# Kernel tuning notes

Hardware: AMD Instinct MI355X
Metric: run time of the kernel (lower is better)

## Reference

```python
import jax, jax.numpy as jnp
import numpy as np


def _pairwise_dist(x):
    # Euclidean (p=2) pairwise distance matrix with a safe sqrt (zero diag).
    sq = jnp.sum(x * x, axis=1)
    d2 = sq[:, None] + sq[None, :] - 2.0 * (x @ x.T)
    d2 = jnp.maximum(d2, 0.0)
    safe = jnp.where(d2 > 0, d2, 1.0)
    return jnp.where(d2 > 0, jnp.sqrt(safe), 0.0)


def _mst_pairs(D):
    # 0-dim Vietoris-Rips persistence pairs == MST edges of the distance graph.
    # Prim's algorithm, vectorized per step via lax.scan (n-1 sequential steps).
    n = D.shape[0]
    D = jax.lax.stop_gradient(D)  # pairing indices are discrete
    inf = jnp.array(jnp.inf, D.dtype)
    idx = jnp.arange(n)
    min_dist = jnp.where(idx == 0, inf, D[0])  # start tree at node 0
    parent = jnp.zeros((n,), dtype=jnp.int32)

    def step(carry, _):
        min_dist, parent = carry
        j = jnp.argmin(min_dist)
        edge = jnp.stack([parent[j], j.astype(jnp.int32)])
        cand = D[j]
        upd = cand < min_dist
        parent = jnp.where(upd, j.astype(jnp.int32), parent)
        min_dist = jnp.minimum(min_dist, cand)
        min_dist = min_dist.at[j].set(inf)
        return (min_dist, parent), edge

    _, edges = jax.lax.scan(step, (min_dist, parent), None, length=n - 1)
    return edges  # [n-1, 2] int32


def setup_inputs() -> dict:
    key = jax.random.key(0)
    kx, kz = jax.random.split(key)
    x = jax.random.normal(kx, (4096, 3072), dtype=jnp.float32)
    z = jax.random.normal(kz, (4096, 128), dtype=jnp.float32)
    return {"x": x, "z": z}


def reference(x, z):
    x = x.astype(jnp.float32)
    z = z.astype(jnp.float32)
    Dx = _pairwise_dist(x)
    Dz = _pairwise_dist(z)
    px = _mst_pairs(Dx)  # persistence pairing of the data space
    pz = _mst_pairs(Dz)  # persistence pairing of the latent space
    dx_px = Dx[px[:, 0], px[:, 1]]
    dz_px = Dz[px[:, 0], px[:, 1]]
    dx_pz = Dx[pz[:, 0], pz[:, 1]]
    dz_pz = Dz[pz[:, 0], pz[:, 1]]
    # Signature matching loss (Moor et al. 2020), p=2:
    # 0.5*||d_X[pi_X] - d_Z[pi_X]||^2 + 0.5*||d_X[pi_Z] - d_Z[pi_Z]||^2
    return 0.5 * jnp.sum((dx_px - dz_px) ** 2) + 0.5 * jnp.sum((dx_pz - dz_pz) ** 2)
```

## Files before the change

kernel.cpp:

```cpp
#include <hip/hip_runtime.h>
#include <hip/hip_fp16.h>

#define N 4096
#define KX 3072
#define KZ 128
#define NBT (N / 128)
#define NTRI2 (NBT * (NBT + 1) / 2)

typedef __attribute__((ext_vector_type(8))) short bf16x8;
typedef __attribute__((ext_vector_type(4))) float f32x4;

__device__ __forceinline__ short f2bf(float f) {
  unsigned u = __float_as_uint(f);
  u += 0x7fffu + ((u >> 16) & 1u);
  return (short)(u >> 16);
}

__device__ __forceinline__ unsigned umin2(unsigned a, unsigned b) { return a < b ? a : b; }

template <int CTRL>
__device__ __forceinline__ unsigned dpp_umin(unsigned x) {
  unsigned y = (unsigned)__builtin_amdgcn_update_dpp(0, (int)x, CTRL, 0xF, 0xF, true);
  return umin2(x, y);
}

__global__ __launch_bounds__(256) void cvt_bf16_kernel(const float* __restrict__ X,
                                                       short* __restrict__ Xb, int n8) {
  int stride = gridDim.x * 256;
  for (int i = blockIdx.x * 256 + threadIdx.x; i < n8; i += stride) {
    float4 a = *(const float4*)(X + (size_t)i * 8);
    float4 b = *(const float4*)(X + (size_t)i * 8 + 4);
    bf16x8 o;
    o[0] = f2bf(a.x); o[1] = f2bf(a.y); o[2] = f2bf(a.z); o[3] = f2bf(a.w);
    o[4] = f2bf(b.x); o[5] = f2bf(b.y); o[6] = f2bf(b.z); o[7] = f2bf(b.w);
    *(bf16x8*)(Xb + (size_t)i * 8) = o;
  }
}

__global__ __launch_bounds__(256) void sqnorm_kernel(const float* __restrict__ X, int K,
                                                     float* __restrict__ sq) {
  int row = blockIdx.x;
  const float4* xr = (const float4*)(X + (size_t)row * K);
  float s = 0.f;
  int n4 = K >> 2;
  for (int i = threadIdx.x; i < n4; i += 256) {
    float4 v = xr[i];
    s += v.x * v.x + v.y * v.y + v.z * v.z + v.w * v.w;
  }
  for (int off = 32; off > 0; off >>= 1) s += __shfl_down(s, off);
  __shared__ float wsum[4];
  int lane = threadIdx.x & 63, w = threadIdx.x >> 6;
  if (lane == 0) wsum[w] = s;
  __syncthreads();
  if (threadIdx.x == 0) {
    float t = 0.f;
    #pragma unroll
    for (int i = 0; i < 4; ++i) t += wsum[i];
    sq[row] = t;
  }
}

__global__ __launch_bounds__(256) void dist_mfma_kernel(const short* __restrict__ Xb, int K,
                                                        const float* __restrict__ sq,
                                                        __half* __restrict__ D) {
  int t = blockIdx.x;
  int br = (int)((sqrtf(8.0f * (float)t + 1.0f) - 1.0f) * 0.5f);
  while ((br + 1) * (br + 2) / 2 <= t) ++br;
  while (br * (br + 1) / 2 > t) --br;
  int bc = t - br * (br + 1) / 2;
  int i0 = br * 128, j0 = bc * 128;

  __shared__ short As[128][40];
  __shared__ short Bs[128][40];

  int tid = threadIdx.x, lane = tid & 63, w = tid >> 6;
  int wr = w >> 1, wc = w & 1;
  int fr = lane & 15, fc = lane >> 4;

  f32x4 acc[4][4];
  #pragma unroll
  for (int m = 0; m < 4; ++m)
    #pragma unroll
    for (int nn = 0; nn < 4; ++nn)
      acc[m][nn] = (f32x4){0.f, 0.f, 0.f, 0.f};

  for (int k0 = 0; k0 < K; k0 += 32) {
    #pragma unroll
    for (int u = 0; u < 2; ++u) {
      int f = tid + u * 256;
      int r = f >> 2;
      int c = (f & 3) * 8;
      *(bf16x8*)&As[r][c] = *(const bf16x8*)(Xb + (size_t)(i0 + r) * K + k0 + c);
      *(bf16x8*)&Bs[r][c] = *(const bf16x8*)(Xb + (size_t)(j0 + r) * K + k0 + c);
    }
    __syncthreads();
    bf16x8 af[4], bg[4];
    #pragma unroll
    for (int m = 0; m < 4; ++m)
      af[m] = *(const bf16x8*)&As[wr * 64 + m * 16 + fr][fc * 8];
    #pragma unroll
    for (int nn = 0; nn < 4; ++nn)
      bg[nn] = *(const bf16x8*)&Bs[wc * 64 + nn * 16 + fr][fc * 8];
    #pragma unroll
    for (int m = 0; m < 4; ++m)
      #pragma unroll
      for (int nn = 0; nn < 4; ++nn)
        acc[m][nn] = __builtin_amdgcn_mfma_f32_16x16x32_bf16(af[m], bg[nn], acc[m][nn], 0, 0, 0);
    __syncthreads();
  }

  #pragma unroll
  for (int m = 0; m < 4; ++m) {
    #pragma unroll
    for (int nn = 0; nn < 4; ++nn) {
      int gj = j0 + wc * 64 + nn * 16 + fr;
      float sqj = sq[gj];
      #pragma unroll
      for (int e = 0; e < 4; ++e) {
        int gi = i0 + wr * 64 + m * 16 + fc * 4 + e;
        float d2 = sq[gi] + sqj - 2.0f * acc[m][nn][e];
        float d = sqrtf(fmaxf(d2, 0.0f));
        __half h = __float2half(d);
        D[(size_t)gi * N + gj] = h;
        D[(size_t)gj * N + gi] = h;
      }
    }
  }
}

#define INFK(idx) (0xFFFF0000u | (unsigned)(idx))

__global__ __launch_bounds__(512) void mst_kernel(const __half* __restrict__ Dx,
                                                  const __half* __restrict__ Dz,
                                                  int2* __restrict__ ex,
                                                  int2* __restrict__ ez) {
  const __half* __restrict__ D = (blockIdx.x == 0) ? Dx : Dz;
  int2* __restrict__ edges = (blockIdx.x == 0) ? ex : ez;

  int tid = threadIdx.x;
  int lane = tid & 63;
  int w = tid >> 6;
  int base = tid * 8;

  unsigned mdk0, mdk1, mdk2, mdk3, mdk4, mdk5, mdk6, mdk7;
  int par0 = 0, par1 = 0, par2 = 0, par3 = 0, par4 = 0, par5 = 0, par6 = 0, par7 = 0;
  {
    uint4 u = *(const uint4*)(D + base);
    mdk0 = (u.x << 16) | (unsigned)(base + 0);
    mdk1 = (u.x & 0xffff0000u) | (unsigned)(base + 1);
    mdk2 = (u.y << 16) | (unsigned)(base + 2);
    mdk3 = (u.y & 0xffff0000u) | (unsigned)(base + 3);
    mdk4 = (u.z << 16) | (unsigned)(base + 4);
    mdk5 = (u.z & 0xffff0000u) | (unsigned)(base + 5);
    mdk6 = (u.w << 16) | (unsigned)(base + 6);
    mdk7 = (u.w & 0xffff0000u) | (unsigned)(base + 7);
  }
  if (tid == 0) mdk0 = INFK(0);

  __shared__ unsigned skey[2][8];
  __shared__ uint2 eld[N - 1];

  int j;
  {
    unsigned x = umin2(umin2(umin2(mdk0, mdk1), umin2(mdk2, mdk3)),
                       umin2(umin2(mdk4, mdk5), umin2(mdk6, mdk7)));
    x = dpp_umin<0xB1>(x);
    x = dpp_umin<0x4E>(x);
    x = dpp_umin<0x141>(x);
    x = dpp_umin<0x140>(x);
    unsigned r0 = (unsigned)__builtin_amdgcn_readlane((int)x, 0);
    unsigned r1 = (unsigned)__builtin_amdgcn_readlane((int)x, 16);
    unsigned r2 = (unsigned)__builtin_amdgcn_readlane((int)x, 32);
    unsigned r3 = (unsigned)__builtin_amdgcn_readlane((int)x, 48);
    unsigned wm = umin2(umin2(r0, r1), umin2(r2, r3));
    if (lane == 0) skey[1][w] = wm;
    __syncthreads();
    uint4 A = ((const uint4*)&skey[1][0])[0];
    uint4 B = ((const uint4*)&skey[1][0])[1];
    unsigned k = umin2(umin2(umin2(A.x, A.y), umin2(A.z, A.w)),
                       umin2(umin2(B.x, B.y), umin2(B.z, B.w)));
    j = (int)(k & 0xFFFu);
  }

  unsigned prk0 = 0xFFFFFFFFu, prk1 = 0xFFFFFFFFu, prk2 = 0xFFFFFFFFu, prk3 = 0xFFFFFFFFu,
           prk4 = 0xFFFFFFFFu, prk5 = 0xFFFFFFFFu, prk6 = 0xFFFFFFFFu, prk7 = 0xFFFFFFFFu;
  int jp = 0, jtprev = -1, jlprev = 0;

  for (int t = 0; t < N - 1; ++t) {
    int p = t & 1;
    int jt = j >> 3, jl = j & 7;

    uint4 u = *(const uint4*)(D + (size_t)j * N + base);
    __builtin_amdgcn_sched_barrier(0);

    #define DUPD(q) { bool up_ = prk##q < mdk##q; mdk##q = up_ ? prk##q : mdk##q; par##q = up_ ? jp : par##q; }
    DUPD(0) DUPD(1) DUPD(2) DUPD(3) DUPD(4) DUPD(5) DUPD(6) DUPD(7)
    #undef DUPD
    if (jtprev == tid) {
      if      (jlprev == 0) mdk0 = INFK(base + 0);
      else if (jlprev == 1) mdk1 = INFK(base + 1);
      else if (jlprev == 2) mdk2 = INFK(base + 2);
      else if (jlprev == 3) mdk3 = INFK(base + 3);
      else if (jlprev == 4) mdk4 = INFK(base + 4);
      else if (jlprev == 5) mdk5 = INFK(base + 5);
      else if (jlprev == 6) mdk6 = INFK(base + 6);
      else                  mdk7 = INFK(base + 7);
    }

    if (jt == tid) {
      int pj = (jl == 0) ? par0 : (jl == 1) ? par1 : (jl == 2) ? par2 :
               (jl == 3) ? par3 : (jl == 4) ? par4 : (jl == 5) ? par5 :
               (jl == 6) ? par6 : par7;
      eld[t] = make_uint2((unsigned)pj, (unsigned)j);
    }

    if (jt == tid) {
      if      (jl == 0) mdk0 = INFK(base + 0);
      else if (jl == 1) mdk1 = INFK(base + 1);
      else if (jl == 2) mdk2 = INFK(base + 2);
      else if (jl == 3) mdk3 = INFK(base + 3);
      else if (jl == 4) mdk4 = INFK(base + 4);
      else if (jl == 5) mdk5 = INFK(base + 5);
      else if (jl == 6) mdk6 = INFK(base + 6);
      else              mdk7 = INFK(base + 7);
    }

    unsigned ak = umin2(umin2(umin2(mdk0, mdk1), umin2(mdk2, mdk3)),
                        umin2(umin2(mdk4, mdk5), umin2(mdk6, mdk7)));

    prk0 = (u.x << 16) | (unsigned)(base + 0);
    prk1 = (u.x & 0xffff0000u) | (unsigned)(base + 1);
    prk2 = (u.y << 16) | (unsigned)(base + 2);
    prk3 = (u.y & 0xffff0000u) | (unsigned)(base + 3);
    prk4 = (u.z << 16) | (unsigned)(base + 4);
    prk5 = (u.z & 0xffff0000u) | (unsigned)(base + 5);
    prk6 = (u.w << 16) | (unsigned)(base + 6);
    prk7 = (u.w & 0xffff0000u) | (unsigned)(base + 7);
    {
      bool self = (jt == tid);
      unsigned b0 = (self && jl == 0) ? 0xFFFFFFFFu : prk0;
      unsigned b1 = (self && jl == 1) ? 0xFFFFFFFFu : prk1;
      unsigned b2 = (self && jl == 2) ? 0xFFFFFFFFu : prk2;
      unsigned b3 = (self && jl == 3) ? 0xFFFFFFFFu : prk3;
      unsigned b4 = (self && jl == 4) ? 0xFFFFFFFFu : prk4;
      unsigned b5 = (self && jl == 5) ? 0xFFFFFFFFu : prk5;
      unsigned b6 = (self && jl == 6) ? 0xFFFFFFFFu : prk6;
      unsigned b7 = (self && jl == 7) ? 0xFFFFFFFFu : prk7;
      unsigned bk = umin2(umin2(umin2(b0, b1), umin2(b2, b3)),
                          umin2(umin2(b4, b5), umin2(b6, b7)));
      unsigned x = umin2(ak, bk);
      x = dpp_umin<0xB1>(x);
      x = dpp_umin<0x4E>(x);
      x = dpp_umin<0x141>(x);
      x = dpp_umin<0x140>(x);
      unsigned r0 = (unsigned)__builtin_amdgcn_readlane((int)x, 0);
      unsigned r1 = (unsigned)__builtin_amdgcn_readlane((int)x, 16);
      unsigned r2 = (unsigned)__builtin_amdgcn_readlane((int)x, 32);
      unsigned r3 = (unsigned)__builtin_amdgcn_readlane((int)x, 48);
      unsigned wm = umin2(umin2(r0, r1), umin2(r2, r3));
      if (lane == 0) skey[p][w] = wm;
    }

    jp = j; jtprev = jt; jlprev = jl;

    __syncthreads();
    uint4 A = ((const uint4*)&skey[p][0])[0];
    uint4 B = ((const uint4*)&skey[p][0])[1];
    unsigned k = umin2(umin2(umin2(A.x, A.y), umin2(A.z, A.w)),
                       umin2(umin2(B.x, B.y), umin2(B.z, B.w)));
    j = (int)(k & 0xFFFu);
  }

  __syncthreads();
  for (int e = tid; e < N - 1; e += 512) {
    uint2 v = eld[e];
    edges[e] = make_int2((int)v.x, (int)v.y);
  }
}

__global__ __launch_bounds__(1024) void loss_kernel(const __half* __restrict__ Dx,
                                                    const __half* __restrict__ Dz,
                                                    const int2* __restrict__ ex,
                                                    const int2* __restrict__ ez,
                                                    float* __restrict__ out) {
  int tid = threadIdx.x;
  float s = 0.f;
  const int M = N - 1;
  for (int e = tid; e < 2 * M; e += 1024) {
    int2 uv = (e < M) ? ex[e] : ez[e - M];
    size_t off = (size_t)uv.x * N + uv.y;
    float dx = __half2float(Dx[off]);
    float dz = __half2float(Dz[off]);
    float d = dx - dz;
    s += d * d;
  }
  for (int off = 32; off > 0; off >>= 1) s += __shfl_down(s, off);
  __shared__ float wsum[16];
  int lane = tid & 63, w = tid >> 6;
  if (lane == 0) wsum[w] = s;
  __syncthreads();
  if (tid == 0) {
    float t = 0.f;
    #pragma unroll
    for (int i = 0; i < 16; ++i) t += wsum[i];
    out[0] = 0.5f * t;
  }
}

extern "C" void kernel_launch(void* const* d_in, const int* in_sizes, int n_in,
                              void* d_out, int out_size, void* d_ws, size_t ws_size,
                              hipStream_t stream) {
  const float* x = (const float*)d_in[0];
  const float* z = (const float*)d_in[1];
  float* out = (float*)d_out;
  char* ws = (char*)d_ws;

  __half* Dx = (__half*)ws;
  __half* Dz = Dx + (size_t)N * N;
  short* Xb = (short*)(Dz + (size_t)N * N);
  short* Zb = Xb + (size_t)N * KX;
  float* sqx = (float*)(Zb + (size_t)N * KZ);
  float* sqz = sqx + N;
  int2* ex = (int2*)(sqz + N);
  int2* ez = ex + (N - 1);

  cvt_bf16_kernel<<<2048, 256, 0, stream>>>(x, Xb, N * KX / 8);
  cvt_bf16_kernel<<<256, 256, 0, stream>>>(z, Zb, N * KZ / 8);
  sqnorm_kernel<<<N, 256, 0, stream>>>(x, KX, sqx);
  sqnorm_kernel<<<N, 256, 0, stream>>>(z, KZ, sqz);
  dist_mfma_kernel<<<NTRI2, 256, 0, stream>>>(Xb, KX, sqx, Dx);
  dist_mfma_kernel<<<NTRI2, 256, 0, stream>>>(Zb, KZ, sqz, Dz);
  mst_kernel<<<2, 512, 0, stream>>>(Dx, Dz, ex, ez);
  loss_kernel<<<1, 1024, 0, stream>>>(Dx, Dz, ex, ez, out);
}
```

Baseline: 2.595 ms.

## Store distance matrices as packed 32-bit half-distance|index keys for MST

The distance kernel can now write each entry as a 32-bit key (fp16 distance bits in the high half, column index in the low half, diagonal set to infinity). The MST kernel then reads ready-made keys instead of building them from half values every step. This removes per-step packing ALU work from the serial Prim loop but doubles the bytes per row read (two 16B loads per thread) and doubles the distance matrix footprint. The key path only runs when the workspace is large enough, otherwise the old half path is used.

```diff
diff --git a/kernel.cpp b/kernel.cpp
--- a/kernel.cpp
+++ b/kernel.cpp
@@ -23,6 +23,8 @@
   unsigned y = (unsigned)__builtin_amdgcn_update_dpp(0, (int)x, CTRL, 0xF, 0xF, true);
   return umin2(x, y);
 }
+
+#define INFK(idx) (0xFFFF0000u | (unsigned)(idx))
 
 __global__ __launch_bounds__(256) void cvt_bf16_kernel(const float* __restrict__ X,
                                                        short* __restrict__ Xb, int n8) {
@@ -60,9 +62,10 @@
   }
 }
 
+template <bool KEYS>
 __global__ __launch_bounds__(256) void dist_mfma_kernel(const short* __restrict__ Xb, int K,
                                                         const float* __restrict__ sq,
-                                                        __half* __restrict__ D) {
+                                                        void* __restrict__ Dout) {
   int t = blockIdx.x;
   int br = (int)((sqrtf(8.0f * (float)t + 1.0f) - 1.0f) * 0.5f);
   while ((br + 1) * (br + 2) / 2 <= t) ++br;
@@ -121,20 +124,28 @@
         float d2 = sq[gi] + sqj - 2.0f * acc[m][nn][e];
         float d = sqrtf(fmaxf(d2, 0.0f));
         __half h = __float2half(d);
-        D[(size_t)gi * N + gj] = h;
-        D[(size_t)gj * N + gi] = h;
+        if constexpr (KEYS) {
+          unsigned hb = (unsigned)__half_as_ushort(h);
+          unsigned* Kd = (unsigned*)Dout;
+          unsigned kij = (gi == gj) ? INFK(gj) : ((hb << 16) | (unsigned)gj);
+          unsigned kji = (gi == gj) ? INFK(gi) : ((hb << 16) | (unsigned)gi);
+          Kd[(size_t)gi * N + gj] = kij;
+          Kd[(size_t)gj * N + gi] = kji;
+        } else {
+          __half* D = (__half*)Dout;
+          D[(size_t)gi * N + gj] = h;
+          D[(size_t)gj * N + gi] = h;
+        }
       }
     }
   }
 }
 
-#define INFK(idx) (0xFFFF0000u | (unsigned)(idx))
-
-__global__ __launch_bounds__(512) void mst_kernel(const __half* __restrict__ Dx,
-                                                  const __half* __restrict__ Dz,
-                                                  int2* __restrict__ ex,
-                                                  int2* __restrict__ ez) {
-  const __half* __restrict__ D = (blockIdx.x == 0) ? Dx : Dz;
+__global__ __launch_bounds__(512) void mst_keys_kernel(const unsigned* __restrict__ Kx,
+                                                       const unsigned* __restrict__ Kz,
+                                                       int2* __restrict__ ex,
+                                                       int2* __restrict__ ez) {
+  const unsigned* __restrict__ Kd = (blockIdx.x == 0) ? Kx : Kz;
   int2* __restrict__ edges = (blockIdx.x == 0) ? ex : ez;
 
   int tid = threadIdx.x;
@@ -145,17 +156,11 @@
   unsigned mdk0, mdk1, mdk2, mdk3, mdk4, mdk5, mdk6, mdk7;
   int par0 = 0, par1 = 0, par2 = 0, par3 = 0, par4 = 0, par5 = 0, par6 = 0, par7 = 0;
   {
-    uint4 u = *(const uint4*)(D + base);
-    mdk0 = (u.x << 16) | (unsigned)(base + 0);
-    mdk1 = (u.x & 0xffff0000u) | (unsigned)(base + 1);
-    mdk2 = (u.y << 16) | (unsigned)(base + 2);
-    mdk3 = (u.y & 0xffff0000u) | (unsigned)(base + 3);
-    mdk4 = (u.z << 16) | (unsigned)(base + 4);
-    mdk5 = (u.z & 0xffff0000u) | (unsigned)(base + 5);
-    mdk6 = (u.w << 16) | (unsigned)(base + 6);
-    mdk7 = (u.w & 0xffff0000u) | (unsigned)(base + 7);
-  }
-  if (tid == 0) mdk0 = INFK(0);
+    uint4 a = *(const uint4*)(Kd + base);
+    uint4 b = *(const uint4*)(Kd + base + 4);
+    mdk0 = a.x; mdk1 = a.y; mdk2 = a.z; mdk3 = a.w;
+    mdk4 = b.x; mdk5 = b.y; mdk6 = b.z; mdk7 = b.w;
+  }
 
   __shared__ unsigned skey[2][8];
   __shared__ uint2 eld[N - 1];
@@ -179,7 +184,142 @@
     uint4 B = ((const uint4*)&skey[1][0])[1];
     unsigned k = umin2(umin2(umin2(A.x, A.y), umin2(A.z, A.w)),
                        umin2(umin2(B.x, B.y), umin2(B.z, B.w)));
-    j = (int)(k & 0xFFFu);
+    j = (int)(k & 0xFFFFu);
+  }
+
+  unsigned prk0 = 0xFFFFFFFFu, prk1 = 0xFFFFFFFFu, prk2 = 0xFFFFFFFFu, prk3 = 0xFFFFFFFFu,
+           prk4 = 0xFFFFFFFFu, prk5 = 0xFFFFFFFFu, prk6 = 0xFFFFFFFFu, prk7 = 0xFFFFFFFFu;
+  int jp = 0, jtprev = -1, jlprev = 0;
+
+  for (int t = 0; t < N - 1; ++t) {
+    int p = t & 1;
+    int jt = j >> 3, jl = j & 7;
+
+    const unsigned* row = Kd + (size_t)j * N + base;
+    uint4 ua = *(const uint4*)row;
+    uint4 ub = *(const uint4*)(row + 4);
+    __builtin_amdgcn_sched_barrier(0);
+
+    #define DUPD(q) { bool up_ = prk##q < mdk##q; mdk##q = up_ ? prk##q : mdk##q; par##q = up_ ? jp : par##q; }
+    DUPD(0) DUPD(1) DUPD(2) DUPD(3) DUPD(4) DUPD(5) DUPD(6) DUPD(7)
+    #undef DUPD
+    if (jtprev == tid) {
+      if      (jlprev == 0) mdk0 = INFK(base + 0);
+      else if (jlprev == 1) mdk1 = INFK(base + 1);
+      else if (jlprev == 2) mdk2 = INFK(base + 2);
+      else if (jlprev == 3) mdk3 = INFK(base + 3);
+      else if (jlprev == 4) mdk4 = INFK(base + 4);
+      else if (jlprev == 5) mdk5 = INFK(base + 5);
+      else if (jlprev == 6) mdk6 = INFK(base + 6);
+      else                  mdk7 = INFK(base + 7);
+    }
+
+    if (jt == tid) {
+      int pj = (jl == 0) ? par0 : (jl == 1) ? par1 : (jl == 2) ? par2 :
+               (jl == 3) ? par3 : (jl == 4) ? par4 : (jl == 5) ? par5 :
+               (jl == 6) ? par6 : par7;
+      eld[t] = make_uint2((unsigned)pj, (unsigned)j);
+    }
+
+    if (jt == tid) {
+      if      (jl == 0) mdk0 = INFK(base + 0);
+      else if (jl == 1) mdk1 = INFK(base + 1);
+      else if (jl == 2) mdk2 = INFK(base + 2);
+      else if (jl == 3) mdk3 = INFK(base + 3);
+      else if (jl == 4) mdk4 = INFK(base + 4);
+      else if (jl == 5) mdk5 = INFK(base + 5);
+      else if (jl == 6) mdk6 = INFK(base + 6);
+      else              mdk7 = INFK(base + 7);
+    }
+
+    unsigned ak = umin2(umin2(umin2(mdk0, mdk1), umin2(mdk2, mdk3)),
+                        umin2(umin2(mdk4, mdk5), umin2(mdk6, mdk7)));
+
+    {
+      unsigned bk = umin2(umin2(umin2(ua.x, ua.y), umin2(ua.z, ua.w)),
+                          umin2(umin2(ub.x, ub.y), umin2(ub.z, ub.w)));
+      unsigned x = umin2(ak, bk);
+      x = dpp_umin<0xB1>(x);
+      x = dpp_umin<0x4E>(x);
+      x = dpp_umin<0x141>(x);
+      x = dpp_umin<0x140>(x);
+      unsigned r0 = (unsigned)__builtin_amdgcn_readlane((int)x, 0);
+      unsigned r1 = (unsigned)__builtin_amdgcn_readlane((int)x, 16);
+      unsigned r2 = (unsigned)__builtin_amdgcn_readlane((int)x, 32);
+      unsigned r3 = (unsigned)__builtin_amdgcn_readlane((int)x, 48);
+      unsigned wm = umin2(umin2(r0, r1), umin2(r2, r3));
+      if (lane == 0) skey[p][w] = wm;
+    }
+
+    prk0 = ua.x; prk1 = ua.y; prk2 = ua.z; prk3 = ua.w;
+    prk4 = ub.x; prk5 = ub.y; prk6 = ub.z; prk7 = ub.w;
+    jp = j; jtprev = jt; jlprev = jl;
+
+    __syncthreads();
+    uint4 A = ((const uint4*)&skey[p][0])[0];
+    uint4 B = ((const uint4*)&skey[p][0])[1];
+    unsigned k = umin2(umin2(umin2(A.x, A.y), umin2(A.z, A.w)),
+                       umin2(umin2(B.x, B.y), umin2(B.z, B.w)));
+    j = (int)(k & 0xFFFFu);
+  }
+
+  __syncthreads();
+  for (int e = tid; e < N - 1; e += 512) {
+    uint2 v = eld[e];
+    edges[e] = make_int2((int)v.x, (int)v.y);
+  }
+}
+
+__global__ __launch_bounds__(512) void mst_half_kernel(const __half* __restrict__ Dx,
+                                                       const __half* __restrict__ Dz,
+                                                       int2* __restrict__ ex,
+                                                       int2* __restrict__ ez) {
+  const __half* __restrict__ D = (blockIdx.x == 0) ? Dx : Dz;
+  int2* __restrict__ edges = (blockIdx.x == 0) ? ex : ez;
+
+  int tid = threadIdx.x;
+  int lane = tid & 63;
+  int w = tid >> 6;
+  int base = tid * 8;
+
+  unsigned mdk0, mdk1, mdk2, mdk3, mdk4, mdk5, mdk6, mdk7;
+  int par0 = 0, par1 = 0, par2 = 0, par3 = 0, par4 = 0, par5 = 0, par6 = 0, par7 = 0;
+  {
+    uint4 u = *(const uint4*)(D + base);
+    mdk0 = (u.x << 16) | (unsigned)(base + 0);
+    mdk1 = (u.x & 0xffff0000u) | (unsigned)(base + 1);
+    mdk2 = (u.y << 16) | (unsigned)(base + 2);
+    mdk3 = (u.y & 0xffff0000u) | (unsigned)(base + 3);
+    mdk4 = (u.z << 16) | (unsigned)(base + 4);
+    mdk5 = (u.z & 0xffff0000u) | (unsigned)(base + 5);
+    mdk6 = (u.w << 16) | (unsigned)(base + 6);
+    mdk7 = (u.w & 0xffff0000u) | (unsigned)(base + 7);
+  }
+  if (tid == 0) mdk0 = INFK(0);
+
+  __shared__ unsigned skey[2][8];
+  __shared__ uint2 eld[N - 1];
+
+  int j;
+  {
+    unsigned x = umin2(umin2(umin2(mdk0, mdk1), umin2(mdk2, mdk3)),
+                       umin2(umin2(mdk4, mdk5), umin2(mdk6, mdk7)));
+    x = dpp_umin<0xB1>(x);
+    x = dpp_umin<0x4E>(x);
+    x = dpp_umin<0x141>(x);
+    x = dpp_umin<0x140>(x);
+    unsigned r0 = (unsigned)__builtin_amdgcn_readlane((int)x, 0);
+    unsigned r1 = (unsigned)__builtin_amdgcn_readlane((int)x, 16);
+    unsigned r2 = (unsigned)__builtin_amdgcn_readlane((int)x, 32);
+    unsigned r3 = (unsigned)__builtin_amdgcn_readlane((int)x, 48);
+    unsigned wm = umin2(umin2(r0, r1), umin2(r2, r3));
+    if (lane == 0) skey[1][w] = wm;
+    __syncthreads();
+    uint4 A = ((const uint4*)&skey[1][0])[0];
+    uint4 B = ((const uint4*)&skey[1][0])[1];
+    unsigned k = umin2(umin2(umin2(A.x, A.y), umin2(A.z, A.w)),
+                       umin2(umin2(B.x, B.y), umin2(B.z, B.w)));
+    j = (int)(k & 0xFFFFu);
   }
 
   unsigned prk0 = 0xFFFFFFFFu, prk1 = 0xFFFFFFFFu, prk2 = 0xFFFFFFFFu, prk3 = 0xFFFFFFFFu,
@@ -268,7 +408,7 @@
     uint4 B = ((const uint4*)&skey[p][0])[1];
     unsigned k = umin2(umin2(umin2(A.x, A.y), umin2(A.z, A.w)),
                        umin2(umin2(B.x, B.y), umin2(B.z, B.w)));
-    j = (int)(k & 0xFFFu);
+    j = (int)(k & 0xFFFFu);
   }
 
   __syncthreads();
@@ -278,8 +418,9 @@
   }
 }
 
-__global__ __launch_bounds__(1024) void loss_kernel(const __half* __restrict__ Dx,
-                                                    const __half* __restrict__ Dz,
+template <bool KEYS>
+__global__ __launch_bounds__(1024) void loss_kernel(const void* __restrict__ DxV,
+                                                    const void* __restrict__ DzV,
                                                     const int2* __restrict__ ex,
                                                     const int2* __restrict__ ez,
                                                     float* __restrict__ out) {
@@ -289,8 +430,14 @@
   for (int e = tid; e < 2 * M; e += 1024) {
     int2 uv = (e < M) ? ex[e] : ez[e - M];
     size_t off = (size_t)uv.x * N + uv.y;
-    float dx = __half2float(Dx[off]);
-    float dz = __half2float(Dz[off]);
+    float dx, dz;
+    if constexpr (KEYS) {
+      dx = __half2float(__ushort_as_half((unsigned short)(((const unsigned*)DxV)[off] >> 16)));
+      dz = __half2float(__ushort_as_half((unsigned short)(((const unsigned*)DzV)[off] >> 16)));
+    } else {
+      dx = __half2float(((const __half*)DxV)[off]);
+      dz = __half2float(((const __half*)DzV)[off]);
+    }
     float d = dx - dz;
     s += d * d;
   }
@@ -315,21 +462,46 @@
   float* out = (float*)d_out;
   char* ws = (char*)d_ws;
 
-  __half* Dx = (__half*)ws;
-  __half* Dz = Dx + (size_t)N * N;
-  short* Xb = (short*)(Dz + (size_t)N * N);
-  short* Zb = Xb + (size_t)N * KX;
-  float* sqx = (float*)(Zb + (size_t)N * KZ);
-  float* sqz = sqx + N;
-  int2* ex = (int2*)(sqz + N);
-  int2* ez = ex + (N - 1);
-
-  cvt_bf16_kernel<<<2048, 256, 0, stream>>>(x, Xb, N * KX / 8);
-  cvt_bf16_kernel<<<256, 256, 0, stream>>>(z, Zb, N * KZ / 8);
-  sqnorm_kernel<<<N, 256, 0, stream>>>(x, KX, sqx);
-  sqnorm_kernel<<<N, 256, 0, stream>>>(z, KZ, sqz);
-  dist_mfma_kernel<<<NTRI2, 256, 0, stream>>>(Xb, KX, sqx, Dx);
-  dist_mfma_kernel<<<NTRI2, 256, 0, stream>>>(Zb, KZ, sqz, Dz);
-  mst_kernel<<<2, 512, 0, stream>>>(Dx, Dz, ex, ez);
-  loss_kernel<<<1, 1024, 0, stream>>>(Dx, Dz, ex, ez, out);
-}
+  size_t need_keys = (size_t)2 * N * N * 4
+                   + (size_t)N * KX * 2 + (size_t)N * KZ * 2
+                   + (size_t)2 * N * 4
+                   + (size_t)2 * (N - 1) * 8;
+
+  if (ws_size >= need_keys) {
+    unsigned* Kx = (unsigned*)ws;
+    unsigned* Kz = Kx + (size_t)N * N;
+    short* Xb = (short*)(Kz + (size_t)N * N);
+    short* Zb = Xb + (size_t)N * KX;
+    float* sqx = (float*)(Zb + (size_t)N * KZ);
+    float* sqz = sqx + N;
+    int2* ex = (int2*)(sqz + N);
+    int2* ez = ex + (N - 1);
+
+    cvt_bf16_kernel<<<2048, 256, 0, stream>>>(x, Xb, N * KX / 8);
+    cvt_bf16_kernel<<<256, 256, 0, stream>>>(z, Zb, N * KZ / 8);
+    sqnorm_kernel<<<N, 256, 0, stream>>>(x, KX, sqx);
+    sqnorm_kernel<<<N, 256, 0, stream>>>(z, KZ, sqz);
+    dist_mfma_kernel<true><<<NTRI2, 256, 0, stream>>>(Xb, KX, sqx, Kx);
+    dist_mfma_kernel<true><<<NTRI2, 256, 0, stream>>>(Zb, KZ, sqz, Kz);
+    mst_keys_kernel<<<2, 512, 0, stream>>>(Kx, Kz, ex, ez);
+    loss_kernel<true><<<1, 1024, 0, stream>>>(Kx, Kz, ex, ez, out);
+  } else {
+    __half* Dx = (__half*)ws;
+    __half* Dz = Dx + (size_t)N * N;
+    short* Xb = (short*)(Dz + (size_t)N * N);
+    short* Zb = Xb + (size_t)N * KX;
+    float* sqx = (float*)(Zb + (size_t)N * KZ);
+    float* sqz = sqx + N;
+    int2* ex = (int2*)(sqz + N);
+    int2* ez = ex + (N - 1);
+
+    cvt_bf16_kernel<<<2048, 256, 0, stream>>>(x, Xb, N * KX / 8);
+    cvt_bf16_kernel<<<256, 256, 0, stream>>>(z, Zb, N * KZ / 8);
+    sqnorm_kernel<<<N, 256, 0, stream>>>(x, KX, sqx);
+    sqnorm_kernel<<<N, 256, 0, stream>>>(z, KZ, sqz);
+    dist_mfma_kernel<false><<<NTRI2, 256, 0, stream>>>(Xb, KX, sqx, Dx);
+    dist_mfma_kernel<false><<<NTRI2, 256, 0, stream>>>(Zb, KZ, sqz, Dz);
+    mst_half_kernel<<<2, 512, 0, stream>>>(Dx, Dz, ex, ez);
+    loss_kernel<false><<<1, 1024, 0, stream>>>(Dx, Dz, ex, ez, out);
+  }
+}
```

Result: faster. 2.225 ms (-14.2%).

## Store packed distance-index keys and split Prim into sequence and parent passes

Applied to the files above, without the earlier changes.

The distance kernel now writes 32-bit keys (fp16 distance in the high half, column index in the low half) so each MST step can find the next vertex with a plain row-min over the new row. This is combined with the running-min array and lets the argmin of step t+1 overlap with the update. Parent tracking moves out of the serial loop into a parallel parent_kernel that replays the visit order over 16 blocks. The cost is twice the memory for the distance matrices, and a fallback to the old half-precision path runs when the workspace is too small.

```diff
diff --git a/kernel.cpp b/kernel.cpp
--- a/kernel.cpp
+++ b/kernel.cpp
@@ -22,6 +22,32 @@
 __device__ __forceinline__ unsigned dpp_umin(unsigned x) {
   unsigned y = (unsigned)__builtin_amdgcn_update_dpp(0, (int)x, CTRL, 0xF, 0xF, true);
   return umin2(x, y);
+}
+
+#define INFK(idx) (0xFFFF0000u | (unsigned)(idx))
+
+__device__ __forceinline__ unsigned rowmin64(const uint4* u) {
+  unsigned bq[16];
+  #pragma unroll
+  for (int q = 0; q < 16; ++q)
+    bq[q] = umin2(umin2(u[q].x, u[q].y), umin2(u[q].z, u[q].w));
+  #pragma unroll
+  for (int s = 8; s; s >>= 1)
+    #pragma unroll
+    for (int q = 0; q < s; ++q) bq[q] = umin2(bq[q], bq[q + s]);
+  return bq[0];
+}
+
+__device__ __forceinline__ unsigned wavemin(unsigned x) {
+  x = dpp_umin<0xB1>(x);
+  x = dpp_umin<0x4E>(x);
+  x = dpp_umin<0x141>(x);
+  x = dpp_umin<0x140>(x);
+  unsigned r0 = (unsigned)__builtin_amdgcn_readlane((int)x, 0);
+  unsigned r1 = (unsigned)__builtin_amdgcn_readlane((int)x, 16);
+  unsigned r2 = (unsigned)__builtin_amdgcn_readlane((int)x, 32);
+  unsigned r3 = (unsigned)__builtin_amdgcn_readlane((int)x, 48);
+  return umin2(umin2(r0, r1), umin2(r2, r3));
 }
 
 __global__ __launch_bounds__(256) void cvt_bf16_kernel(const float* __restrict__ X,
@@ -60,9 +86,10 @@
   }
 }
 
+template <bool KEYS>
 __global__ __launch_bounds__(256) void dist_mfma_kernel(const short* __restrict__ Xb, int K,
                                                         const float* __restrict__ sq,
-                                                        __half* __restrict__ D) {
+                                                        void* __restrict__ Dout) {
   int t = blockIdx.x;
   int br = (int)((sqrtf(8.0f * (float)t + 1.0f) - 1.0f) * 0.5f);
   while ((br + 1) * (br + 2) / 2 <= t) ++br;
@@ -121,19 +148,138 @@
         float d2 = sq[gi] + sqj - 2.0f * acc[m][nn][e];
         float d = sqrtf(fmaxf(d2, 0.0f));
         __half h = __float2half(d);
-        D[(size_t)gi * N + gj] = h;
-        D[(size_t)gj * N + gi] = h;
+        if constexpr (KEYS) {
+          unsigned hb = (unsigned)__half_as_ushort(h);
+          unsigned* Kd = (unsigned*)Dout;
+          unsigned kij = (gi == gj) ? INFK(gj) : ((hb << 16) | (unsigned)gj);
+          unsigned kji = (gi == gj) ? INFK(gi) : ((hb << 16) | (unsigned)gi);
+          Kd[(size_t)gi * N + gj] = kij;
+          Kd[(size_t)gj * N + gi] = kji;
+        } else {
+          __half* D = (__half*)Dout;
+          D[(size_t)gi * N + gj] = h;
+          D[(size_t)gj * N + gi] = h;
+        }
       }
     }
   }
 }
 
-#define INFK(idx) (0xFFFF0000u | (unsigned)(idx))
-
-__global__ __launch_bounds__(512) void mst_kernel(const __half* __restrict__ Dx,
-                                                  const __half* __restrict__ Dz,
-                                                  int2* __restrict__ ex,
-                                                  int2* __restrict__ ez) {
+__global__ __launch_bounds__(512) void mst_seq_kernel(const unsigned* __restrict__ Kx,
+                                                      const unsigned* __restrict__ Kz,
+                                                      unsigned* __restrict__ seqx,
+                                                      unsigned* __restrict__ seqz) {
+  const unsigned* __restrict__ Kd = (blockIdx.x == 0) ? Kx : Kz;
+  unsigned* __restrict__ seqo = (blockIdx.x == 0) ? seqx : seqz;
+
+  int tid = threadIdx.x, lane = tid & 63, w = tid >> 6;
+  unsigned ob0 = (unsigned)((2 * w) * 256 + lane * 4);
+  unsigned ob1 = ob0 + 256;
+
+  __shared__ unsigned skey[2][8];
+  __shared__ unsigned seqlds[N - 1];
+
+  unsigned mdk[8];
+  unsigned j;
+  {
+    uint4 u[16];
+    #pragma unroll
+    for (int q = 0; q < 16; ++q)
+      u[q] = *(const uint4*)(Kd + q * 256 + lane * 4);
+    uint4 v0 = *(const uint4*)(Kd + ob0);
+    uint4 v1 = *(const uint4*)(Kd + ob1);
+    unsigned key = wavemin(rowmin64(u));
+    j = key & 0xFFFFu;
+    mdk[0] = v0.x; mdk[1] = v0.y; mdk[2] = v0.z; mdk[3] = v0.w;
+    mdk[4] = v1.x; mdk[5] = v1.y; mdk[6] = v1.z; mdk[7] = v1.w;
+  }
+
+  unsigned prk[8];
+  #pragma unroll
+  for (int k = 0; k < 8; ++k) prk[k] = 0xFFFFFFFFu;
+  unsigned jprev = 0xFFFFFFFFu;
+
+  for (int t = 0; t < N - 1; ++t) {
+    int p = t & 1;
+
+    const unsigned* row = Kd + (size_t)j * N;
+    uint4 u[16];
+    #pragma unroll
+    for (int q = 0; q < 16; ++q)
+      u[q] = *(const uint4*)(row + q * 256 + lane * 4);
+    uint4 v0 = *(const uint4*)(row + ob0);
+    uint4 v1 = *(const uint4*)(row + ob1);
+    __builtin_amdgcn_sched_barrier(0);
+
+    #pragma unroll
+    for (int k = 0; k < 8; ++k) {
+      unsigned idx = (k < 4) ? (ob0 + (unsigned)k) : (ob1 + (unsigned)(k - 4));
+      unsigned m = umin2(mdk[k], prk[k]);
+      m = (idx == jprev) ? INFK(idx) : m;
+      m = (idx == j) ? INFK(idx) : m;
+      mdk[k] = m;
+    }
+    {
+      unsigned a = umin2(umin2(umin2(mdk[0], mdk[1]), umin2(mdk[2], mdk[3])),
+                         umin2(umin2(mdk[4], mdk[5]), umin2(mdk[6], mdk[7])));
+      unsigned aw = wavemin(a);
+      if (lane == 0) skey[p][w] = aw;
+    }
+    if (tid == 0) seqlds[t] = j;
+
+    asm volatile("s_waitcnt lgkmcnt(0)\n\ts_barrier" ::: "memory");
+
+    uint4 A0 = ((const uint4*)&skey[p][0])[0];
+    uint4 A1 = ((const uint4*)&skey[p][0])[1];
+    unsigned ag = umin2(umin2(umin2(A0.x, A0.y), umin2(A0.z, A0.w)),
+                        umin2(umin2(A1.x, A1.y), umin2(A1.z, A1.w)));
+
+    unsigned bg = wavemin(rowmin64(u));
+
+    unsigned key = umin2(ag, bg);
+    jprev = j;
+    j = key & 0xFFFFu;
+    prk[0] = v0.x; prk[1] = v0.y; prk[2] = v0.z; prk[3] = v0.w;
+    prk[4] = v1.x; prk[5] = v1.y; prk[6] = v1.z; prk[7] = v1.w;
+  }
+
+  __syncthreads();
+  for (int e = tid; e < N - 1; e += 512) seqo[e] = seqlds[e];
+}
+
+__global__ __launch_bounds__(512) void parent_kernel(const unsigned* __restrict__ Kx,
+                                                     const unsigned* __restrict__ Kz,
+                                                     const unsigned* __restrict__ seqx,
+                                                     const unsigned* __restrict__ seqz,
+                                                     int2* __restrict__ ex,
+                                                     int2* __restrict__ ez) {
+  int b = blockIdx.x;
+  bool isz = (b >= 8);
+  const unsigned* __restrict__ Kd = isz ? Kz : Kx;
+  const unsigned* __restrict__ seq = isz ? seqz : seqx;
+  int2* __restrict__ edges = isz ? ez : ex;
+  unsigned wn = (unsigned)(((b & 7) * 512) + threadIdx.x);
+
+  __shared__ unsigned sseq[N - 1];
+  for (int i = threadIdx.x; i < N - 1; i += 512) sseq[i] = seq[i];
+  __syncthreads();
+
+  unsigned md = Kd[wn];
+  int par = 0;
+  #pragma unroll 4
+  for (int t = 0; t < N - 1; ++t) {
+    unsigned r = sseq[t];
+    if (r == wn) edges[t] = make_int2(par, (int)wn);
+    unsigned v = Kd[(size_t)r * N + wn];
+    if (v < md) { md = v; par = (int)r; }
+    if (r == wn) md = 0xFFFFFFFFu;
+  }
+}
+
+__global__ __launch_bounds__(512) void mst_half_kernel(const __half* __restrict__ Dx,
+                                                       const __half* __restrict__ Dz,
+                                                       int2* __restrict__ ex,
+                                                       int2* __restrict__ ez) {
   const __half* __restrict__ D = (blockIdx.x == 0) ? Dx : Dz;
   int2* __restrict__ edges = (blockIdx.x == 0) ? ex : ez;
 
@@ -164,22 +310,14 @@
   {
     unsigned x = umin2(umin2(umin2(mdk0, mdk1), umin2(mdk2, mdk3)),
                        umin2(umin2(mdk4, mdk5), umin2(mdk6, mdk7)));
-    x = dpp_umin<0xB1>(x);
-    x = dpp_umin<0x4E>(x);
-    x = dpp_umin<0x141>(x);
-    x = dpp_umin<0x140>(x);
-    unsigned r0 = (unsigned)__builtin_amdgcn_readlane((int)x, 0);
-    unsigned r1 = (unsigned)__builtin_amdgcn_readlane((int)x, 16);
-    unsigned r2 = (unsigned)__builtin_amdgcn_readlane((int)x, 32);
-    unsigned r3 = (unsigned)__builtin_amdgcn_readlane((int)x, 48);
-    unsigned wm = umin2(umin2(r0, r1), umin2(r2, r3));
+    unsigned wm = wavemin(x);
     if (lane == 0) skey[1][w] = wm;
     __syncthreads();
     uint4 A = ((const uint4*)&skey[1][0])[0];
     uint4 B = ((const uint4*)&skey[1][0])[1];
     unsigned k = umin2(umin2(umin2(A.x, A.y), umin2(A.z, A.w)),
                        umin2(umin2(B.x, B.y), umin2(B.z, B.w)));
-    j = (int)(k & 0xFFFu);
+    j = (int)(k & 0xFFFFu);
   }
 
   unsigned prk0 = 0xFFFFFFFFu, prk1 = 0xFFFFFFFFu, prk2 = 0xFFFFFFFFu, prk3 = 0xFFFFFFFFu,
@@ -248,16 +386,7 @@
       unsigned b7 = (self && jl == 7) ? 0xFFFFFFFFu : prk7;
       unsigned bk = umin2(umin2(umin2(b0, b1), umin2(b2, b3)),
                           umin2(umin2(b4, b5), umin2(b6, b7)));
-      unsigned x = umin2(ak, bk);
-      x = dpp_umin<0xB1>(x);
-      x = dpp_umin<0x4E>(x);
-      x = dpp_umin<0x141>(x);
-      x = dpp_umin<0x140>(x);
-      unsigned r0 = (unsigned)__builtin_amdgcn_readlane((int)x, 0);
-      unsigned r1 = (unsigned)__builtin_amdgcn_readlane((int)x, 16);
-      unsigned r2 = (unsigned)__builtin_amdgcn_readlane((int)x, 32);
-      unsigned r3 = (unsigned)__builtin_amdgcn_readlane((int)x, 48);
-      unsigned wm = umin2(umin2(r0, r1), umin2(r2, r3));
+      unsigned wm = wavemin(umin2(ak, bk));
       if (lane == 0) skey[p][w] = wm;
     }
 
@@ -268,7 +397,7 @@
     uint4 B = ((const uint4*)&skey[p][0])[1];
     unsigned k = umin2(umin2(umin2(A.x, A.y), umin2(A.z, A.w)),
                        umin2(umin2(B.x, B.y), umin2(B.z, B.w)));
-    j = (int)(k & 0xFFFu);
+    j = (int)(k & 0xFFFFu);
   }
 
   __syncthreads();
@@ -278,8 +407,9 @@
   }
 }
 
-__global__ __launch_bounds__(1024) void loss_kernel(const __half* __restrict__ Dx,
-                                                    const __half* __restrict__ Dz,
+template <bool KEYS>
+__global__ __launch_bounds__(1024) void loss_kernel(const void* __restrict__ DxV,
+                                                    const void* __restrict__ DzV,
                                                     const int2* __restrict__ ex,
                                                     const int2* __restrict__ ez,
                                                     float* __restrict__ out) {
@@ -289,8 +419,14 @@
   for (int e = tid; e < 2 * M; e += 1024) {
     int2 uv = (e < M) ? ex[e] : ez[e - M];
     size_t off = (size_t)uv.x * N + uv.y;
-    float dx = __half2float(Dx[off]);
-    float dz = __half2float(Dz[off]);
+    float dx, dz;
+    if constexpr (KEYS) {
+      dx = __half2float(__ushort_as_half((unsigned short)(((const unsigned*)DxV)[off] >> 16)));
+      dz = __half2float(__ushort_as_half((unsigned short)(((const unsigned*)DzV)[off] >> 16)));
+    } else {
+      dx = __half2float(((const __half*)DxV)[off]);
+      dz = __half2float(((const __half*)DzV)[off]);
+    }
     float d = dx - dz;
     s += d * d;
   }
@@ -315,21 +451,49 @@
   float* out = (float*)d_out;
   char* ws = (char*)d_ws;
 
-  __half* Dx = (__half*)ws;
-  __half* Dz = Dx + (size_t)N * N;
-  short* Xb = (short*)(Dz + (size_t)N * N);
-  short* Zb = Xb + (size_t)N * KX;
-  float* sqx = (float*)(Zb + (size_t)N * KZ);
-  float* sqz = sqx + N;
-  int2* ex = (int2*)(sqz + N);
-  int2* ez = ex + (N - 1);
-
-  cvt_bf16_kernel<<<2048, 256, 0, stream>>>(x, Xb, N * KX / 8);
-  cvt_bf16_kernel<<<256, 256, 0, stream>>>(z, Zb, N * KZ / 8);
-  sqnorm_kernel<<<N, 256, 0, stream>>>(x, KX, sqx);
-  sqnorm_kernel<<<N, 256, 0, stream>>>(z, KZ, sqz);
-  dist_mfma_kernel<<<NTRI2, 256, 0, stream>>>(Xb, KX, sqx, Dx);
-  dist_mfma_kernel<<<NTRI2, 256, 0, stream>>>(Zb, KZ, sqz, Dz);
-  mst_kernel<<<2, 512, 0, stream>>>(Dx, Dz, ex, ez);
-  loss_kernel<<<1, 1024, 0, stream>>>(Dx, Dz, ex, ez, out);
-}
+  size_t need_keys = (size_t)2 * N * N * 4
+                   + (size_t)N * KX * 2 + (size_t)N * KZ * 2
+                   + (size_t)2 * N * 4
+                   + (size_t)2 * (N - 1) * 8;
+
+  if (ws_size >= need_keys) {
+    unsigned* Kx = (unsigned*)ws;
+    unsigned* Kz = Kx + (size_t)N * N;
+    short* Xb = (short*)(Kz + (size_t)N * N);
+    short* Zb = Xb + (size_t)N * KX;
+    float* sqx = (float*)(Zb + (size_t)N * KZ);
+    float* sqz = sqx + N;
+    int2* ex = (int2*)(sqz + N);
+    int2* ez = ex + (N - 1);
+    unsigned* seqx = (unsigned*)Xb;
+    unsigned* seqz = seqx + (N - 1);
+
+    cvt_bf16_kernel<<<2048, 256, 0, stream>>>(x, Xb, N * KX / 8);
+    cvt_bf16_kernel<<<256, 256, 0, stream>>>(z, Zb, N * KZ / 8);
+    sqnorm_kernel<<<N, 256, 0, stream>>>(x, KX, sqx);
+    sqnorm_kernel<<<N, 256, 0, stream>>>(z, KZ, sqz);
+    dist_mfma_kernel<true><<<NTRI2, 256, 0, stream>>>(Xb, KX, sqx, Kx);
+    dist_mfma_kernel<true><<<NTRI2, 256, 0, stream>>>(Zb, KZ, sqz, Kz);
+    mst_seq_kernel<<<2, 512, 0, stream>>>(Kx, Kz, seqx, seqz);
+    parent_kernel<<<16, 512, 0, stream>>>(Kx, Kz, seqx, seqz, ex, ez);
+    loss_kernel<true><<<1, 1024, 0, stream>>>(Kx, Kz, ex, ez, out);
+  } else {
+    __half* Dx = (__half*)ws;
+    __half* Dz = Dx + (size_t)N * N;
+    short* Xb = (short*)(Dz + (size_t)N * N);
+    short* Zb = Xb + (size_t)N * KX;
+    float* sqx = (float*)(Zb + (size_t)N * KZ);
+    float* sqz = sqx + N;
+    int2* ex = (int2*)(sqz + N);
+    int2* ez = ex + (N - 1);
+
+    cvt_bf16_kernel<<<2048, 256, 0, stream>>>(x, Xb, N * KX / 8);
+    cvt_bf16_kernel<<<256, 256, 0, stream>>>(z, Zb, N * KZ / 8);
+    sqnorm_kernel<<<N, 256, 0, stream>>>(x, KX, sqx);
+    sqnorm_kernel<<<N, 256, 0, stream>>>(z, KZ, sqz);
+    dist_mfma_kernel<false><<<NTRI2, 256, 0, stream>>>(Xb, KX, sqx, Dx);
+    dist_mfma_kernel<false><<<NTRI2, 256, 0, stream>>>(Zb, KZ, sqz, Dz);
+    mst_half_kernel<<<2, 512, 0, stream>>>(Dx, Dz, ex, ez);
+    loss_kernel<false><<<1, 1024, 0, stream>>>(Dx, Dz, ex, ez, out);
+  }
+}
```

After: 6.059 ms. 134% more time.

## Store precomputed 32-bit (distance,index) keys in matrix to shorten MST inner loop

Applied to the files above, without the earlier changes.

The distance kernel now writes packed 32-bit keys (fp16 distance bits in the high half, column index in the low half, diagonal set to infinity) instead of plain fp16 distances. The serial Prim loop then loads keys directly and skips the per-step packing and self-masking ALU work. The cost is that the matrices double in size, so each row fetch in the latency-bound MST loop reads twice as many bytes and the distance kernel's stores double. The loss kernel extracts the fp16 from the high bits.

```diff
diff --git a/kernel.cpp b/kernel.cpp
--- a/kernel.cpp
+++ b/kernel.cpp
@@ -23,6 +23,8 @@
   unsigned y = (unsigned)__builtin_amdgcn_update_dpp(0, (int)x, CTRL, 0xF, 0xF, true);
   return umin2(x, y);
 }
+
+#define INFK(idx) (0xFFFF0000u | (unsigned)(idx))
 
 __global__ __launch_bounds__(256) void cvt_bf16_kernel(const float* __restrict__ X,
                                                        short* __restrict__ Xb, int n8) {
@@ -62,7 +64,7 @@
 
 __global__ __launch_bounds__(256) void dist_mfma_kernel(const short* __restrict__ Xb, int K,
                                                         const float* __restrict__ sq,
-                                                        __half* __restrict__ D) {
+                                                        unsigned* __restrict__ Kd) {
   int t = blockIdx.x;
   int br = (int)((sqrtf(8.0f * (float)t + 1.0f) - 1.0f) * 0.5f);
   while ((br + 1) * (br + 2) / 2 <= t) ++br;
@@ -120,21 +122,21 @@
         int gi = i0 + wr * 64 + m * 16 + fc * 4 + e;
         float d2 = sq[gi] + sqj - 2.0f * acc[m][nn][e];
         float d = sqrtf(fmaxf(d2, 0.0f));
-        __half h = __float2half(d);
-        D[(size_t)gi * N + gj] = h;
-        D[(size_t)gj * N + gi] = h;
+        unsigned hb = (unsigned)__half_as_ushort(__float2half(d));
+        unsigned kij = (gi == gj) ? INFK(gj) : ((hb << 16) | (unsigned)gj);
+        unsigned kji = (gi == gj) ? INFK(gi) : ((hb << 16) | (unsigned)gi);
+        Kd[(size_t)gi * N + gj] = kij;
+        Kd[(size_t)gj * N + gi] = kji;
       }
     }
   }
 }
 
-#define INFK(idx) (0xFFFF0000u | (unsigned)(idx))
-
-__global__ __launch_bounds__(512) void mst_kernel(const __half* __restrict__ Dx,
-                                                  const __half* __restrict__ Dz,
-                                                  int2* __restrict__ ex,
-                                                  int2* __restrict__ ez) {
-  const __half* __restrict__ D = (blockIdx.x == 0) ? Dx : Dz;
+__global__ __launch_bounds__(512) void mst_keys_kernel(const unsigned* __restrict__ Kx,
+                                                       const unsigned* __restrict__ Kz,
+                                                       int2* __restrict__ ex,
+                                                       int2* __restrict__ ez) {
+  const unsigned* __restrict__ Kd = (blockIdx.x == 0) ? Kx : Kz;
   int2* __restrict__ edges = (blockIdx.x == 0) ? ex : ez;
 
   int tid = threadIdx.x;
@@ -145,17 +147,11 @@
   unsigned mdk0, mdk1, mdk2, mdk3, mdk4, mdk5, mdk6, mdk7;
   int par0 = 0, par1 = 0, par2 = 0, par3 = 0, par4 = 0, par5 = 0, par6 = 0, par7 = 0;
   {
-    uint4 u = *(const uint4*)(D + base);
-    mdk0 = (u.x << 16) | (unsigned)(base + 0);
-    mdk1 = (u.x & 0xffff0000u) | (unsigned)(base + 1);
-    mdk2 = (u.y << 16) | (unsigned)(base + 2);
-    mdk3 = (u.y & 0xffff0000u) | (unsigned)(base + 3);
-    mdk4 = (u.z << 16) | (unsigned)(base + 4);
-    mdk5 = (u.z & 0xffff0000u) | (unsigned)(base + 5);
-    mdk6 = (u.w << 16) | (unsigned)(base + 6);
-    mdk7 = (u.w & 0xffff0000u) | (unsigned)(base + 7);
-  }
-  if (tid == 0) mdk0 = INFK(0);
+    uint4 a = *(const uint4*)(Kd + base);
+    uint4 b = *(const uint4*)(Kd + base + 4);
+    mdk0 = a.x; mdk1 = a.y; mdk2 = a.z; mdk3 = a.w;
+    mdk4 = b.x; mdk5 = b.y; mdk6 = b.z; mdk7 = b.w;
+  }
 
   __shared__ unsigned skey[2][8];
   __shared__ uint2 eld[N - 1];
@@ -179,7 +175,7 @@
     uint4 B = ((const uint4*)&skey[1][0])[1];
     unsigned k = umin2(umin2(umin2(A.x, A.y), umin2(A.z, A.w)),
                        umin2(umin2(B.x, B.y), umin2(B.z, B.w)));
-    j = (int)(k & 0xFFFu);
+    j = (int)(k & 0xFFFFu);
   }
 
   unsigned prk0 = 0xFFFFFFFFu, prk1 = 0xFFFFFFFFu, prk2 = 0xFFFFFFFFu, prk3 = 0xFFFFFFFFu,
@@ -190,7 +186,9 @@
     int p = t & 1;
     int jt = j >> 3, jl = j & 7;
 
-    uint4 u = *(const uint4*)(D + (size_t)j * N + base);
+    const unsigned* row = Kd + (size_t)j * N + base;
+    uint4 ua = *(const uint4*)row;
+    uint4 ub = *(const uint4*)(row + 4);
     __builtin_amdgcn_sched_barrier(0);
 
     #define DUPD(q) { bool up_ = prk##q < mdk##q; mdk##q = up_ ? prk##q : mdk##q; par##q = up_ ? jp : par##q; }
@@ -228,26 +226,9 @@
     unsigned ak = umin2(umin2(umin2(mdk0, mdk1), umin2(mdk2, mdk3)),
                         umin2(umin2(mdk4, mdk5), umin2(mdk6, mdk7)));
 
-    prk0 = (u.x << 16) | (unsigned)(base + 0);
-    prk1 = (u.x & 0xffff0000u) | (unsigned)(base + 1);
-    prk2 = (u.y << 16) | (unsigned)(base + 2);
-    prk3 = (u.y & 0xffff0000u) | (unsigned)(base + 3);
-    prk4 = (u.z << 16) | (unsigned)(base + 4);
-    prk5 = (u.z & 0xffff0000u) | (unsigned)(base + 5);
-    prk6 = (u.w << 16) | (unsigned)(base + 6);
-    prk7 = (u.w & 0xffff0000u) | (unsigned)(base + 7);
     {
-      bool self = (jt == tid);
-      unsigned b0 = (self && jl == 0) ? 0xFFFFFFFFu : prk0;
-      unsigned b1 = (self && jl == 1) ? 0xFFFFFFFFu : prk1;
-      unsigned b2 = (self && jl == 2) ? 0xFFFFFFFFu : prk2;
-      unsigned b3 = (self && jl == 3) ? 0xFFFFFFFFu : prk3;
-      unsigned b4 = (self && jl == 4) ? 0xFFFFFFFFu : prk4;
-      unsigned b5 = (self && jl == 5) ? 0xFFFFFFFFu : prk5;
-      unsigned b6 = (self && jl == 6) ? 0xFFFFFFFFu : prk6;
-      unsigned b7 = (self && jl == 7) ? 0xFFFFFFFFu : prk7;
-      unsigned bk = umin2(umin2(umin2(b0, b1), umin2(b2, b3)),
-                          umin2(umin2(b4, b5), umin2(b6, b7)));
+      unsigned bk = umin2(umin2(umin2(ua.x, ua.y), umin2(ua.z, ua.w)),
+                          umin2(umin2(ub.x, ub.y), umin2(ub.z, ub.w)));
       unsigned x = umin2(ak, bk);
       x = dpp_umin<0xB1>(x);
       x = dpp_umin<0x4E>(x);
@@ -261,6 +242,8 @@
       if (lane == 0) skey[p][w] = wm;
     }
 
+    prk0 = ua.x; prk1 = ua.y; prk2 = ua.z; prk3 = ua.w;
+    prk4 = ub.x; prk5 = ub.y; prk6 = ub.z; prk7 = ub.w;
     jp = j; jtprev = jt; jlprev = jl;
 
     __syncthreads();
@@ -268,7 +251,7 @@
     uint4 B = ((const uint4*)&skey[p][0])[1];
     unsigned k = umin2(umin2(umin2(A.x, A.y), umin2(A.z, A.w)),
                        umin2(umin2(B.x, B.y), umin2(B.z, B.w)));
-    j = (int)(k & 0xFFFu);
+    j = (int)(k & 0xFFFFu);
   }
 
   __syncthreads();
@@ -278,8 +261,8 @@
   }
 }
 
-__global__ __launch_bounds__(1024) void loss_kernel(const __half* __restrict__ Dx,
-                                                    const __half* __restrict__ Dz,
+__global__ __launch_bounds__(1024) void loss_kernel(const unsigned* __restrict__ KxM,
+                                                    const unsigned* __restrict__ KzM,
                                                     const int2* __restrict__ ex,
                                                     const int2* __restrict__ ez,
                                                     float* __restrict__ out) {
@@ -289,8 +272,8 @@
   for (int e = tid; e < 2 * M; e += 1024) {
     int2 uv = (e < M) ? ex[e] : ez[e - M];
     size_t off = (size_t)uv.x * N + uv.y;
-    float dx = __half2float(Dx[off]);
-    float dz = __half2float(Dz[off]);
+    float dx = __half2float(__ushort_as_half((unsigned short)(KxM[off] >> 16)));
+    float dz = __half2float(__ushort_as_half((unsigned short)(KzM[off] >> 16)));
     float d = dx - dz;
     s += d * d;
   }
@@ -315,9 +298,9 @@
   float* out = (float*)d_out;
   char* ws = (char*)d_ws;
 
-  __half* Dx = (__half*)ws;
-  __half* Dz = Dx + (size_t)N * N;
-  short* Xb = (short*)(Dz + (size_t)N * N);
+  unsigned* Kx = (unsigned*)ws;
+  unsigned* Kz = Kx + (size_t)N * N;
+  short* Xb = (short*)(Kz + (size_t)N * N);
   short* Zb = Xb + (size_t)N * KX;
   float* sqx = (float*)(Zb + (size_t)N * KZ);
   float* sqz = sqx + N;
@@ -328,8 +311,8 @@
   cvt_bf16_kernel<<<256, 256, 0, stream>>>(z, Zb, N * KZ / 8);
   sqnorm_kernel<<<N, 256, 0, stream>>>(x, KX, sqx);
   sqnorm_kernel<<<N, 256, 0, stream>>>(z, KZ, sqz);
-  dist_mfma_kernel<<<NTRI2, 256, 0, stream>>>(Xb, KX, sqx, Dx);
-  dist_mfma_kernel<<<NTRI2, 256, 0, stream>>>(Zb, KZ, sqz, Dz);
-  mst_kernel<<<2, 512, 0, stream>>>(Dx, Dz, ex, ez);
-  loss_kernel<<<1, 1024, 0, stream>>>(Dx, Dz, ex, ez, out);
-}
+  dist_mfma_kernel<<<NTRI2, 256, 0, stream>>>(Xb, KX, sqx, Kx);
+  dist_mfma_kernel<<<NTRI2, 256, 0, stream>>>(Zb, KZ, sqz, Kz);
+  mst_keys_kernel<<<2, 512, 0, stream>>>(Kx, Kz, ex, ez);
+  loss_kernel<<<1, 1024, 0, stream>>>(Kx, Kz, ex, ez, out);
+}
```

New measurement: 2.225 ms. 14.2% less time.
